# Kernel optimization log

Measured on AMD Instinct MI355X. Metric: run time of the kernel, lower is better.

Reference implementation:

```python
import jax, jax.numpy as jnp
import numpy as np

V, E, H, B, S = 50257, 1024, 1024, 32, 1024

def setup_inputs() -> dict:
    key = jax.random.key(0)
    ks = jax.random.split(key, 16)
    s = 0.02
    return {
        "word_inputs": jax.random.randint(ks[0], (B, 1), 0, V),
        "hidden": jax.random.normal(ks[1], (1, B, H), jnp.float32),
        "output_encoder": jax.random.normal(ks[2], (B, S, H), jnp.float32),
        "emb": jax.random.normal(ks[3], (V, E), jnp.float32) * 0.2,
        "W_a1": jax.random.normal(ks[4], (H, 2 * H), jnp.float32) * s,
        "b_a1": jnp.zeros((H,), jnp.float32),
        "W_a2": jax.random.normal(ks[5], (1, H), jnp.float32) * s,
        "b_a2": jnp.zeros((1,), jnp.float32),
        "W_c": jax.random.normal(ks[6], (H, 2 * H), jnp.float32) * s,
        "b_c": jnp.zeros((H,), jnp.float32),
        "W_ih": jax.random.normal(ks[7], (3 * H, E), jnp.float32) * s,
        "W_hh": jax.random.normal(ks[8], (3 * H, H), jnp.float32) * s,
        "b_ih": jnp.zeros((3 * H,), jnp.float32),
        "b_hh": jnp.zeros((3 * H,), jnp.float32),
        "W_fc": jax.random.normal(ks[9], (V, H), jnp.float32) * 0.2,
        "b_fc": jnp.zeros((V,), jnp.float32),
    }

def reference(word_inputs, hidden, output_encoder, emb, W_a1, b_a1, W_a2, b_a2,
              W_c, b_c, W_ih, W_hh, b_ih, b_hh, W_fc, b_fc):
    b, s, h = output_encoder.shape
    h_prev = hidden[0]                                      # [B,H]
    # Bahdanau additive attention, vectorized over all S timesteps
    eh = jnp.concatenate(
        [output_encoder, jnp.broadcast_to(h_prev[:, None, :], (b, s, h))],
        axis=-1)                                            # [B,S,2H]
    scores = jnp.tanh(jnp.einsum('bsk,hk->bsh', eh, W_a1) + b_a1)
    scores = (jnp.einsum('bsh,oh->bso', scores, W_a2) + b_a2)[..., 0]  # [B,S]
    attn = jax.nn.softmax(scores, axis=1)                   # [B,S]
    context = jnp.einsum('bs,bsh->bh', attn, output_encoder)  # [B,H]
    embedded = emb[word_inputs.reshape(-1)]                 # [B,E]
    ec = jnp.concatenate([embedded, context], axis=-1)      # [B,E+H]
    x = jax.nn.relu(ec @ W_c.T + b_c)                       # [B,H]
    # single-step GRU (PyTorch gate order: r, z, n)
    gi = x @ W_ih.T + b_ih                                  # [B,3H]
    gh = h_prev @ W_hh.T + b_hh                             # [B,3H]
    i_r, i_z, i_n = jnp.split(gi, 3, axis=-1)
    h_r, h_z, h_n = jnp.split(gh, 3, axis=-1)
    r = jax.nn.sigmoid(i_r + h_r)
    z = jax.nn.sigmoid(i_z + h_z)
    n = jnp.tanh(i_n + r * h_n)
    h_new = (1.0 - z) * n + z * h_prev                      # [B,H]
    out = jax.nn.relu(h_new) @ W_fc.T + b_fc                # [B,V]
    return out, h_new[None, :, :]
```

## Files before the change

### kernel.cpp

```cpp
#include <hip/hip_runtime.h>

#define B_  32
#define S_  1024
#define H_  1024
#define V_  50257

typedef __attribute__((ext_vector_type(8))) short bf16x8;
typedef __attribute__((ext_vector_type(4))) float f32x4;
typedef __attribute__((ext_vector_type(8))) unsigned short u16x8;

__device__ __forceinline__ unsigned short f2b(float f) {
  union { float f; unsigned u; } v; v.f = f;
  unsigned r = 0x7FFFu + ((v.u >> 16) & 1u);
  return (unsigned short)((v.u + r) >> 16);
}
__device__ __forceinline__ float b2f(unsigned short h) {
  union { unsigned u; float f; } v; v.u = ((unsigned)h) << 16;
  return v.f;
}

__device__ __forceinline__ void async16(void* lds, const void* g) {
  typedef __attribute__((address_space(3))) void as3_void;
  typedef __attribute__((address_space(1))) void as1_void;
  as3_void* l = (as3_void*)(unsigned)(unsigned long long)lds;
  const as1_void* s = (const as1_void*)(unsigned long long)g;
  __builtin_amdgcn_global_load_lds(s, l, 16, 0, 0);
}

__global__ void conv_f32_bf16(const float* __restrict__ src, unsigned short* __restrict__ dst) {
  size_t i = ((size_t)blockIdx.x * 256 + threadIdx.x) * 8;
  float4 v0 = *(const float4*)(src + i);
  float4 v1 = *(const float4*)(src + i + 4);
  u16x8 o;
  o[0]=f2b(v0.x); o[1]=f2b(v0.y); o[2]=f2b(v0.z); o[3]=f2b(v0.w);
  o[4]=f2b(v1.x); o[5]=f2b(v1.y); o[6]=f2b(v1.z); o[7]=f2b(v1.w);
  *(u16x8*)(dst + i) = o;
}

__global__ void wa1_prep_kernel(const float* __restrict__ wa1, const float* __restrict__ hidden,
                                const float* __restrict__ b_a1,
                                unsigned short* __restrict__ wa1_bf, float* __restrict__ part2) {
  int h = blockIdx.x;
  int tid = threadIdx.x;
  {
    int c = tid * 4;
    float4 v = *(const float4*)(wa1 + (size_t)h * 2048 + c);
    ushort4 o;
    o.x = f2b(v.x); o.y = f2b(v.y); o.z = f2b(v.z); o.w = f2b(v.w);
    *(ushort4*)(wa1_bf + (size_t)h * 1024 + c) = o;
  }
  __shared__ float wrow[H_];
  {
    int c = tid * 4;
    float4 v = *(const float4*)(wa1 + (size_t)h * 2048 + 1024 + c);
    wrow[c] = v.x; wrow[c+1] = v.y; wrow[c+2] = v.z; wrow[c+3] = v.w;
  }
  __syncthreads();
  int wave = tid >> 6, lane = tid & 63;
  float bias = b_a1[h];
  for (int bb = 0; bb < 8; ++bb) {
    int b = wave * 8 + bb;
    float acc = 0.f;
    for (int k = lane; k < H_; k += 64) acc += wrow[k] * hidden[b * H_ + k];
    #pragma unroll
    for (int off = 32; off; off >>= 1) acc += __shfl_xor(acc, off);
    if (lane == 0) part2[b * H_ + h] = acc + bias;
  }
}

#define NT_ 16
#define BAR()  __builtin_amdgcn_s_barrier()
#define SB0()  __builtin_amdgcn_sched_barrier(0)
#define VM6()  asm volatile("s_waitcnt vmcnt(6)" ::: "memory")
#define VM0()  asm volatile("s_waitcnt vmcnt(0)" ::: "memory")

#define LOADA(MH) { _Pragma("unroll") for (int m_ = 0; m_ < 4; ++m_) \
  { _Pragma("unroll") for (int ks_ = 0; ks_ < 2; ++ks_) { \
    int lr_ = (MH)*64 + m_*16 + l15; \
    int lin_ = lr_*128 + ks_*64 + l16*16; \
    int sw_ = lin_ ^ (((lin_>>9)&1)<<5); \
    af[m_][ks_] = *(const bf16x8*)(smem + buf*32768 + wr*16384 + sw_); } } }

#define LOADB() { _Pragma("unroll") for (int n_ = 0; n_ < 4; ++n_) \
  { _Pragma("unroll") for (int ks_ = 0; ks_ < 2; ++ks_) { \
    int lr_ = (wc&1)*64 + n_*16 + l15; \
    int lin_ = lr_*128 + ks_*64 + l16*16; \
    int sw_ = lin_ ^ (((lin_>>9)&1)<<5); \
    bfr[n_][ks_] = *(const bf16x8*)(smem + 65536 + buf*32768 + (wc>>1)*16384 + sw_); } } }

#define QUAD(MH, NH) { _Pragma("unroll") for (int m_ = 0; m_ < 4; ++m_) \
  { _Pragma("unroll") for (int n_ = 0; n_ < 2; ++n_) { \
    acc[(MH)*4+m_][(NH)*2+n_] = __builtin_amdgcn_mfma_f32_16x16x32_bf16(af[m_][0], bfr[(NH)*2+n_][0], acc[(MH)*4+m_][(NH)*2+n_], 0,0,0); \
    acc[(MH)*4+m_][(NH)*2+n_] = __builtin_amdgcn_mfma_f32_16x16x32_bf16(af[m_][1], bfr[(NH)*2+n_][1], acc[(MH)*4+m_][(NH)*2+n_], 0,0,0); } } }

#define PHASES(T, DO_B1, DO_T2, VMOP) { \
  const int buf = (T) & 1; \
  LOADA(0); LOADB(); \
  if (DO_B1) stB((T)+1, 1, buf^1); \
  BAR(); SB0(); \
  __builtin_amdgcn_s_setprio(1); QUAD(0,0); __builtin_amdgcn_s_setprio(0); \
  SB0(); BAR(); \
  if (DO_T2) stB((T)+2, 0, buf); \
  BAR(); SB0(); \
  __builtin_amdgcn_s_setprio(1); QUAD(0,1); __builtin_amdgcn_s_setprio(0); \
  SB0(); BAR(); \
  LOADA(1); \
  BAR(); SB0(); \
  __builtin_amdgcn_s_setprio(1); QUAD(1,1); __builtin_amdgcn_s_setprio(0); \
  SB0(); BAR(); \
  if (DO_T2) { stA((T)+2, 0, buf); stA((T)+2, 1, buf); } \
  VMOP; \
  BAR(); SB0(); \
  __builtin_amdgcn_s_setprio(1); QUAD(1,0); __builtin_amdgcn_s_setprio(0); \
  SB0(); BAR(); }

__global__ __launch_bounds__(512, 2) void scores_gemm8(
    const unsigned short* __restrict__ A,
    const unsigned short* __restrict__ Bm,
    const float* __restrict__ part2,
    const float* __restrict__ wa2,
    float* __restrict__ partials)
{
  extern __shared__ char smem[];
  const int tid = threadIdx.x;
  const int wave = tid >> 6, lane = tid & 63;
  const int wr = wave >> 2, wc = wave & 3;
  const int l15 = lane & 15, l16 = lane >> 4;
  const int bm = blockIdx.x, bn = blockIdx.y;

  const unsigned short* Abase = A  + (size_t)(bm * 256) * 1024;
  const unsigned short* Bbase = Bm + (size_t)(bn * 256) * 1024;

  const int Lc = tid * 16;
  const int Ls = Lc ^ (((Lc >> 9) & 1) << 5);
  const int sr = Ls >> 7;
  const int sk = (Ls & 127) >> 1;

  auto stA = [&](int t, int h, int db) {
    char* dst = smem + db * 32768 + h * 16384 + Lc;
    const unsigned short* src = Abase + (size_t)(h * 128 + sr) * 1024 + t * 64 + sk;
    async16(dst,        src);
    async16(dst + 8192, src + 64 * 1024);
  };
  auto stB = [&](int t, int h, int db) {
    char* dst = smem + 65536 + db * 32768 + h * 16384 + Lc;
    const unsigned short* src = Bbase + (size_t)(h * 128 + sr) * 1024 + t * 64 + sk;
    async16(dst,        src);
    async16(dst + 8192, src + 64 * 1024);
  };

  f32x4 acc[8][4];
  #pragma unroll
  for (int i = 0; i < 8; ++i)
    #pragma unroll
    for (int j = 0; j < 4; ++j) acc[i][j] = (f32x4){0.f, 0.f, 0.f, 0.f};
  bf16x8 af[4][2], bfr[4][2];

  stA(0, 0, 0); stA(0, 1, 0); stB(0, 0, 0); stB(0, 1, 0);
  stB(1, 0, 1); stA(1, 0, 1); stA(1, 1, 1);
  VM6();
  BAR();

  #pragma unroll 1
  for (int t = 0; t < NT_ - 2; ++t) PHASES(t, 1, 1, VM6());
  PHASES(NT_ - 2, 1, 0, VM0());
  PHASES(NT_ - 1, 0, 0, (void)0);

  const int b = bm >> 2;
  float w2[4], p2[4];
  #pragma unroll
  for (int ni = 0; ni < 4; ++ni) {
    int col = bn * 256 + wc * 64 + ni * 16 + l15;
    w2[ni] = wa2[col];
    p2[ni] = part2[b * H_ + col];
  }
  #pragma unroll
  for (int mi = 0; mi < 8; ++mi) {
    #pragma unroll
    for (int r = 0; r < 4; ++r) {
      float s = 0.f;
      #pragma unroll
      for (int ni = 0; ni < 4; ++ni)
        s += w2[ni] * tanhf(acc[mi][ni][r] + p2[ni]);
      s += __shfl_xor(s, 1); s += __shfl_xor(s, 2);
      s += __shfl_xor(s, 4); s += __shfl_xor(s, 8);
      if (l15 == 0) {
        int row = bm * 256 + wr * 128 + mi * 16 + l16 * 4 + r;
        partials[(size_t)row * 16 + bn * 4 + wc] = s;
      }
    }
  }
}

__global__ void softmax_kernel(const float* __restrict__ partials, const float* __restrict__ b_a2,
                               float* __restrict__ attn) {
  int b = blockIdx.x, s = threadIdx.x;
  int lane = s & 63, wid = s >> 6;
  const float4* p = (const float4*)(partials + (size_t)(b * S_ + s) * 16);
  float sc = b_a2[0];
  #pragma unroll
  for (int i = 0; i < 4; ++i) { float4 v = p[i]; sc += v.x + v.y + v.z + v.w; }
  __shared__ float rmax[16], rsum[16];
  float m = sc;
  #pragma unroll
  for (int off = 32; off; off >>= 1) m = fmaxf(m, __shfl_xor(m, off));
  if (lane == 0) rmax[wid] = m;
  __syncthreads();
  float M = rmax[0];
  #pragma unroll
  for (int i = 1; i < 16; ++i) M = fmaxf(M, rmax[i]);
  float e = expf(sc - M);
  float su = e;
  #pragma unroll
  for (int off = 32; off; off >>= 1) su += __shfl_xor(su, off);
  if (lane == 0) rsum[wid] = su;
  __syncthreads();
  float T = 0.f;
  #pragma unroll
  for (int i = 0; i < 16; ++i) T += rsum[i];
  attn[b * S_ + s] = e / T;
}

__global__ void ctx_partial_kernel(const unsigned short* __restrict__ encbf,
                                   const float* __restrict__ attn, float* __restrict__ ctxp) {
  int sc = blockIdx.x, b = blockIdx.y, t = threadIdx.x;
  int h4 = t * 4;
  float a0 = 0, a1 = 0, a2 = 0, a3 = 0;
  const unsigned short* base = encbf + (size_t)b * S_ * H_ + h4;
  const float* aw = attn + b * S_ + sc * 64;
  #pragma unroll 4
  for (int i = 0; i < 64; ++i) {
    float w = aw[i];
    ushort4 ev = *(const ushort4*)(base + (size_t)(sc * 64 + i) * H_);
    a0 += w * b2f(ev.x); a1 += w * b2f(ev.y); a2 += w * b2f(ev.z); a3 += w * b2f(ev.w);
  }
  float4 o = {a0, a1, a2, a3};
  *(float4*)(ctxp + (size_t)(sc * B_ + b) * H_ + h4) = o;
}

__global__ void prep_kernel(const float* __restrict__ ctxp, const float* __restrict__ emb,
                            const int* __restrict__ word, const float* __restrict__ hidden,
                            unsigned short* __restrict__ ec_bf, unsigned short* __restrict__ hprev_bf) {
  int b = blockIdx.x;
  int w = word[b];
  for (int h = threadIdx.x; h < H_; h += 256) {
    float c = 0.f;
    #pragma unroll
    for (int sc = 0; sc < 16; ++sc) c += ctxp[(size_t)(sc * B_ + b) * H_ + h];
    ec_bf[b * 2048 + 1024 + h] = f2b(c);
    ec_bf[b * 2048 + h] = f2b(emb[(size_t)w * H_ + h]);
    hprev_bf[b * H_ + h] = f2b(hidden[b * H_ + h]);
  }
}

__global__ __launch_bounds__(256) void skinny_gemm(
    const unsigned short* __restrict__ A, const float* __restrict__ Bw,
    float* __restrict__ C, const float* __restrict__ bias,
    int N, int K, int KC, int ldc, int mode)
{
  int n0 = blockIdx.x * 64;
  int kc = blockIdx.y;
  int wave = threadIdx.x >> 6, lane = threadIdx.x & 63;
  int l15 = lane & 15, l16 = lane >> 4;
  int col = n0 + wave * 16 + l15;
  int vclamp = col < N ? col : N - 1;
  const unsigned short* a0p = A + l15 * K + l16 * 8;
  const unsigned short* a1p = A + (16 + l15) * K + l16 * 8;
  const float* bp = Bw + (size_t)vclamp * K + l16 * 8;
  f32x4 acc0 = {0.f, 0.f, 0.f, 0.f}, acc1 = {0.f, 0.f, 0.f, 0.f};
  int k0 = kc * KC, k1 = (k0 + KC < K) ? (k0 + KC) : K;
  #pragma unroll 4
  for (int k = k0; k < k1; k += 32) {
    bf16x8 a0 = *(const bf16x8*)(a0p + k);
    bf16x8 a1 = *(const bf16x8*)(a1p + k);
    float4 bv0 = *(const float4*)(bp + k);
    float4 bv1 = *(const float4*)(bp + k + 4);
    bf16x8 bb;
    bb[0] = (short)f2b(bv0.x); bb[1] = (short)f2b(bv0.y);
    bb[2] = (short)f2b(bv0.z); bb[3] = (short)f2b(bv0.w);
    bb[4] = (short)f2b(bv1.x); bb[5] = (short)f2b(bv1.y);
    bb[6] = (short)f2b(bv1.z); bb[7] = (short)f2b(bv1.w);
    acc0 = __builtin_amdgcn_mfma_f32_16x16x32_bf16(a0, bb, acc0, 0, 0, 0);
    acc1 = __builtin_amdgcn_mfma_f32_16x16x32_bf16(a1, bb, acc1, 0, 0, 0);
  }
  if (col < N) {
    #pragma unroll
    for (int r = 0; r < 4; ++r) {
      int m = l16 * 4 + r;
      if (mode == 1) {
        float bv = bias[col];
        C[(size_t)m * ldc + col] = acc0[r] + bv;
        C[(size_t)(16 + m) * ldc + col] = acc1[r] + bv;
      } else {
        C[(size_t)(kc * 32 + m) * N + col] = acc0[r];
        C[(size_t)(kc * 32 + 16 + m) * N + col] = acc1[r];
      }
    }
  }
}

__global__ __launch_bounds__(256) void ihhh_gemm(
    const unsigned short* __restrict__ x_bf, const unsigned short* __restrict__ hprev_bf,
    const float* __restrict__ W_ih, const float* __restrict__ W_hh,
    float* __restrict__ gip, float* __restrict__ ghp)
{
  const unsigned short* A = blockIdx.z ? hprev_bf : x_bf;
  const float* Bw = blockIdx.z ? W_hh : W_ih;
  float* C = blockIdx.z ? ghp : gip;
  const int N = 3072, K = 1024, KC = 128;
  int n0 = blockIdx.x * 64;
  int kc = blockIdx.y;
  int wave = threadIdx.x >> 6, lane = threadIdx.x & 63;
  int l15 = lane & 15, l16 = lane >> 4;
  int col = n0 + wave * 16 + l15;
  const unsigned short* a0p = A + l15 * K + l16 * 8;
  const unsigned short* a1p = A + (16 + l15) * K + l16 * 8;
  const float* bp = Bw + (size_t)col * K + l16 * 8;
  f32x4 acc0 = {0.f, 0.f, 0.f, 0.f}, acc1 = {0.f, 0.f, 0.f, 0.f};
  int k0 = kc * KC;
  #pragma unroll 4
  for (int k = k0; k < k0 + KC; k += 32) {
    bf16x8 a0 = *(const bf16x8*)(a0p + k);
    bf16x8 a1 = *(const bf16x8*)(a1p + k);
    float4 bv0 = *(const float4*)(bp + k);
    float4 bv1 = *(const float4*)(bp + k + 4);
    bf16x8 bb;
    bb[0] = (short)f2b(bv0.x); bb[1] = (short)f2b(bv0.y);
    bb[2] = (short)f2b(bv0.z); bb[3] = (short)f2b(bv0.w);
    bb[4] = (short)f2b(bv1.x); bb[5] = (short)f2b(bv1.y);
    bb[6] = (short)f2b(bv1.z); bb[7] = (short)f2b(bv1.w);
    acc0 = __builtin_amdgcn_mfma_f32_16x16x32_bf16(a0, bb, acc0, 0, 0, 0);
    acc1 = __builtin_amdgcn_mfma_f32_16x16x32_bf16(a1, bb, acc1, 0, 0, 0);
  }
  #pragma unroll
  for (int r = 0; r < 4; ++r) {
    int m = l16 * 4 + r;
    C[(size_t)(kc * 32 + m) * N + col] = acc0[r];
    C[(size_t)(kc * 32 + 16 + m) * N + col] = acc1[r];
  }
}

__global__ void xfinish_kernel(const float* __restrict__ xp, const float* __restrict__ b_c,
                               unsigned short* __restrict__ x_bf) {
  int i = blockIdx.x * 256 + threadIdx.x;
  int b = i >> 10, h = i & 1023;
  float v = b_c[h];
  #pragma unroll
  for (int kc = 0; kc < 16; ++kc) v += xp[(size_t)(kc * B_ + b) * H_ + h];
  x_bf[i] = f2b(v > 0.f ? v : 0.f);
}

__global__ void gates_kernel(const float* __restrict__ gip, const float* __restrict__ ghp,
                             const float* __restrict__ b_ih, const float* __restrict__ b_hh,
                             const float* __restrict__ hidden, float* __restrict__ hnew_out,
                             unsigned short* __restrict__ hr_bf) {
  int i = blockIdx.x * 256 + threadIdx.x;
  int b = i >> 10, h = i & 1023;
  float g[6];
  #pragma unroll
  for (int t = 0; t < 3; ++t) {
    int j = h + t * H_;
    float vi = b_ih[j], vh = b_hh[j];
    #pragma unroll
    for (int kc = 0; kc < 8; ++kc) {
      vi += gip[(size_t)(kc * B_ + b) * 3072 + j];
      vh += ghp[(size_t)(kc * B_ + b) * 3072 + j];
    }
    g[t] = vi; g[3 + t] = vh;
  }
  float r = 1.f / (1.f + expf(-(g[0] + g[3])));
  float z = 1.f / (1.f + expf(-(g[1] + g[4])));
  float n = tanhf(g[2] + r * g[5]);
  float hv = (1.f - z) * n + z * hidden[i];
  hnew_out[i] = hv;
  hr_bf[i] = f2b(hv > 0.f ? hv : 0.f);
}

extern "C" void kernel_launch(void* const* d_in, const int* in_sizes, int n_in,
                              void* d_out, int out_size, void* d_ws, size_t ws_size,
                              hipStream_t stream) {
  const int*   word   = (const int*)  d_in[0];
  const float* hidden = (const float*)d_in[1];
  const float* enc    = (const float*)d_in[2];
  const float* emb    = (const float*)d_in[3];
  const float* W_a1   = (const float*)d_in[4];
  const float* b_a1   = (const float*)d_in[5];
  const float* W_a2   = (const float*)d_in[6];
  const float* b_a2   = (const float*)d_in[7];
  const float* W_c    = (const float*)d_in[8];
  const float* b_c    = (const float*)d_in[9];
  const float* W_ih   = (const float*)d_in[10];
  const float* W_hh   = (const float*)d_in[11];
  const float* b_ih   = (const float*)d_in[12];
  const float* b_hh   = (const float*)d_in[13];
  const float* W_fc   = (const float*)d_in[14];
  const float* b_fc   = (const float*)d_in[15];
  float* out = (float*)d_out;

  if (ws_size < 71892992ull) return;

  char* ws = (char*)d_ws;
  unsigned short* enc_bf   = (unsigned short*)(ws + 0);
  float*          gip      = (float*)         (ws + 0);
  float*          ghp      = (float*)         (ws + 3145728);
  unsigned short* wa1_bf   = (unsigned short*)(ws + 67108864);
  float*          xp       = (float*)         (ws + 67108864);
  float*          part2    = (float*)         (ws + 69206016);
  float*          partials = (float*)         (ws + 69337088);
  float*          ctxp     = (float*)         (ws + 69337088);
  float*          attn     = (float*)         (ws + 71434240);
  unsigned short* ec_bf    = (unsigned short*)(ws + 71565312);
  unsigned short* hprev_bf = (unsigned short*)(ws + 71696384);
  unsigned short* x_bf     = (unsigned short*)(ws + 71761920);
  unsigned short* hr_bf    = (unsigned short*)(ws + 71827456);

  hipFuncSetAttribute((const void*)scores_gemm8,
                      hipFuncAttributeMaxDynamicSharedMemorySize, 131072);

  conv_f32_bf16<<<dim3(16384), dim3(256), 0, stream>>>(enc, enc_bf);
  wa1_prep_kernel<<<dim3(1024), dim3(256), 0, stream>>>(W_a1, hidden, b_a1, wa1_bf, part2);
  scores_gemm8<<<dim3(128, 4), dim3(512), 131072, stream>>>(enc_bf, wa1_bf, part2, W_a2, partials);
  softmax_kernel<<<dim3(32), dim3(1024), 0, stream>>>(partials, b_a2, attn);
  ctx_partial_kernel<<<dim3(16, 32), dim3(256), 0, stream>>>(enc_bf, attn, ctxp);
  prep_kernel<<<dim3(32), dim3(256), 0, stream>>>(ctxp, emb, word, hidden, ec_bf, hprev_bf);
  skinny_gemm<<<dim3(16, 16), dim3(256), 0, stream>>>(ec_bf, W_c, xp, (const float*)nullptr,
                                                      1024, 2048, 128, 0, 0);
  xfinish_kernel<<<dim3(128), dim3(256), 0, stream>>>(xp, b_c, x_bf);
  ihhh_gemm<<<dim3(48, 8, 2), dim3(256), 0, stream>>>(x_bf, hprev_bf, W_ih, W_hh, gip, ghp);
  gates_kernel<<<dim3(128), dim3(256), 0, stream>>>(gip, ghp, b_ih, b_hh, hidden,
                                                    out + (size_t)B_ * V_, hr_bf);
  skinny_gemm<<<dim3(786, 1), dim3(256), 0, stream>>>(hr_bf, W_fc, out, b_fc,
                                                      V_, 1024, 1024, V_, 1);
}
```

Baseline: 288.2 us.

## Fuse prologue, softmax+context, operand prep and bias/relu into fewer GEMM kernels

Merges the encoder bf16 conversion and W_a1 prep into one launch. Softmax is recomputed inside each context block instead of running as a separate kernel. The context-partial reduction and embedding gather move into the W_c GEMM's LDS staging, and the W_c partial reduction with bias and relu moves into the ih/hh GEMM staging. This removes four kernel launches and their intermediate buffers, at the cost of repeating the softmax and partial-sum reductions in many blocks, which adds L2 read traffic.

```diff
diff --git a/kernel.cpp b/kernel.cpp
--- a/kernel.cpp
+++ b/kernel.cpp
@@ -27,21 +27,23 @@
   __builtin_amdgcn_global_load_lds(s, l, 16, 0, 0);
 }
 
-__global__ void conv_f32_bf16(const float* __restrict__ src, unsigned short* __restrict__ dst) {
-  size_t i = ((size_t)blockIdx.x * 256 + threadIdx.x) * 8;
-  float4 v0 = *(const float4*)(src + i);
-  float4 v1 = *(const float4*)(src + i + 4);
-  u16x8 o;
-  o[0]=f2b(v0.x); o[1]=f2b(v0.y); o[2]=f2b(v0.z); o[3]=f2b(v0.w);
-  o[4]=f2b(v1.x); o[5]=f2b(v1.y); o[6]=f2b(v1.z); o[7]=f2b(v1.w);
-  *(u16x8*)(dst + i) = o;
-}
-
-__global__ void wa1_prep_kernel(const float* __restrict__ wa1, const float* __restrict__ hidden,
+__global__ void prologue_kernel(const float* __restrict__ enc, unsigned short* __restrict__ enc_bf,
+                                const float* __restrict__ wa1, const float* __restrict__ hidden,
                                 const float* __restrict__ b_a1,
                                 unsigned short* __restrict__ wa1_bf, float* __restrict__ part2) {
-  int h = blockIdx.x;
+  __shared__ float wrow[H_];
   int tid = threadIdx.x;
+  if (blockIdx.x < 16384) {
+    size_t i = ((size_t)blockIdx.x * 256 + tid) * 8;
+    float4 v0 = *(const float4*)(enc + i);
+    float4 v1 = *(const float4*)(enc + i + 4);
+    u16x8 o;
+    o[0]=f2b(v0.x); o[1]=f2b(v0.y); o[2]=f2b(v0.z); o[3]=f2b(v0.w);
+    o[4]=f2b(v1.x); o[5]=f2b(v1.y); o[6]=f2b(v1.z); o[7]=f2b(v1.w);
+    *(u16x8*)(enc_bf + i) = o;
+    return;
+  }
+  int h = blockIdx.x - 16384;
   {
     int c = tid * 4;
     float4 v = *(const float4*)(wa1 + (size_t)h * 2048 + c);
@@ -49,7 +51,6 @@
     o.x = f2b(v.x); o.y = f2b(v.y); o.z = f2b(v.z); o.w = f2b(v.w);
     *(ushort4*)(wa1_bf + (size_t)h * 1024 + c) = o;
   }
-  __shared__ float wrow[H_];
   {
     int c = tid * 4;
     float4 v = *(const float4*)(wa1 + (size_t)h * 2048 + 1024 + c);
@@ -192,45 +193,44 @@
   }
 }
 
-__global__ void softmax_kernel(const float* __restrict__ partials, const float* __restrict__ b_a2,
-                               float* __restrict__ attn) {
-  int b = blockIdx.x, s = threadIdx.x;
-  int lane = s & 63, wid = s >> 6;
-  const float4* p = (const float4*)(partials + (size_t)(b * S_ + s) * 16);
-  float sc = b_a2[0];
-  #pragma unroll
-  for (int i = 0; i < 4; ++i) { float4 v = p[i]; sc += v.x + v.y + v.z + v.w; }
-  __shared__ float rmax[16], rsum[16];
-  float m = sc;
-  #pragma unroll
-  for (int off = 32; off; off >>= 1) m = fmaxf(m, __shfl_xor(m, off));
-  if (lane == 0) rmax[wid] = m;
-  __syncthreads();
-  float M = rmax[0];
-  #pragma unroll
-  for (int i = 1; i < 16; ++i) M = fmaxf(M, rmax[i]);
-  float e = expf(sc - M);
-  float su = e;
-  #pragma unroll
-  for (int off = 32; off; off >>= 1) su += __shfl_xor(su, off);
-  if (lane == 0) rsum[wid] = su;
-  __syncthreads();
-  float T = 0.f;
-  #pragma unroll
-  for (int i = 0; i < 16; ++i) T += rsum[i];
-  attn[b * S_ + s] = e / T;
-}
-
-__global__ void ctx_partial_kernel(const unsigned short* __restrict__ encbf,
-                                   const float* __restrict__ attn, float* __restrict__ ctxp) {
-  int sc = blockIdx.x, b = blockIdx.y, t = threadIdx.x;
-  int h4 = t * 4;
+__global__ __launch_bounds__(256) void smctx_kernel(
+    const float* __restrict__ partials, const unsigned short* __restrict__ encbf,
+    float* __restrict__ ctxp) {
+  int sc = blockIdx.x, b = blockIdx.y, tid = threadIdx.x;
+  int lane = tid & 63, wid = tid >> 6;
+  __shared__ float att[1024];
+  __shared__ float red[4];
+  float scv[4];
+  float mx = -1e30f;
+  #pragma unroll
+  for (int j = 0; j < 4; ++j) {
+    int r = tid * 4 + j;
+    const float4* p = (const float4*)(partials + ((size_t)b * 1024 + r) * 16);
+    float s = 0.f;
+    #pragma unroll
+    for (int i = 0; i < 4; ++i) { float4 v = p[i]; s += v.x + v.y + v.z + v.w; }
+    scv[j] = s; mx = fmaxf(mx, s);
+  }
+  #pragma unroll
+  for (int off = 32; off; off >>= 1) mx = fmaxf(mx, __shfl_xor(mx, off));
+  if (lane == 0) red[wid] = mx;
+  __syncthreads();
+  float M = fmaxf(fmaxf(red[0], red[1]), fmaxf(red[2], red[3]));
+  float ssum = 0.f;
+  #pragma unroll
+  for (int j = 0; j < 4; ++j) { float e = expf(scv[j] - M); att[tid*4+j] = e; ssum += e; }
+  #pragma unroll
+  for (int off = 32; off; off >>= 1) ssum += __shfl_xor(ssum, off);
+  __syncthreads();
+  if (lane == 0) red[wid] = ssum;
+  __syncthreads();
+  float inv = 1.f / (red[0] + red[1] + red[2] + red[3]);
+  int h4 = tid * 4;
   float a0 = 0, a1 = 0, a2 = 0, a3 = 0;
   const unsigned short* base = encbf + (size_t)b * S_ * H_ + h4;
-  const float* aw = attn + b * S_ + sc * 64;
   #pragma unroll 4
   for (int i = 0; i < 64; ++i) {
-    float w = aw[i];
+    float w = att[sc * 64 + i] * inv;
     ushort4 ev = *(const ushort4*)(base + (size_t)(sc * 64 + i) * H_);
     a0 += w * b2f(ev.x); a1 += w * b2f(ev.y); a2 += w * b2f(ev.z); a3 += w * b2f(ev.w);
   }
@@ -238,28 +238,161 @@
   *(float4*)(ctxp + (size_t)(sc * B_ + b) * H_ + h4) = o;
 }
 
-__global__ void prep_kernel(const float* __restrict__ ctxp, const float* __restrict__ emb,
-                            const int* __restrict__ word, const float* __restrict__ hidden,
-                            unsigned short* __restrict__ ec_bf, unsigned short* __restrict__ hprev_bf) {
-  int b = blockIdx.x;
-  int w = word[b];
-  for (int h = threadIdx.x; h < H_; h += 256) {
-    float c = 0.f;
-    #pragma unroll
-    for (int sc = 0; sc < 16; ++sc) c += ctxp[(size_t)(sc * B_ + b) * H_ + h];
-    ec_bf[b * 2048 + 1024 + h] = f2b(c);
-    ec_bf[b * 2048 + h] = f2b(emb[(size_t)w * H_ + h]);
-    hprev_bf[b * H_ + h] = f2b(hidden[b * H_ + h]);
-  }
-}
-
-__global__ __launch_bounds__(256) void skinny_gemm(
+__global__ __launch_bounds__(256) void wc_gemm(
+    const int* __restrict__ word, const float* __restrict__ emb,
+    const float* __restrict__ ctxp, const float* __restrict__ Wc,
+    float* __restrict__ xp) {
+  int nb = blockIdx.x, kc = blockIdx.y, tid = threadIdx.x;
+  __shared__ unsigned short A_lds[32][136];
+  {
+    int b = tid >> 3, cg = tid & 7;
+    int c0 = cg * 16;
+    if (kc < 8) {
+      int w = word[b];
+      const float* er = emb + (size_t)w * H_ + kc * 128 + c0;
+      #pragma unroll
+      for (int c = 0; c < 16; c += 4) {
+        float4 v = *(const float4*)(er + c);
+        ushort4 o; o.x = f2b(v.x); o.y = f2b(v.y); o.z = f2b(v.z); o.w = f2b(v.w);
+        *(ushort4*)&A_lds[b][c0 + c] = o;
+      }
+    } else {
+      int h0 = (kc - 8) * 128 + c0;
+      #pragma unroll
+      for (int c = 0; c < 16; c += 4) {
+        float s0 = 0, s1 = 0, s2 = 0, s3 = 0;
+        #pragma unroll
+        for (int sc = 0; sc < 16; ++sc) {
+          float4 v = *(const float4*)(ctxp + ((size_t)(sc * B_ + b)) * H_ + h0 + c);
+          s0 += v.x; s1 += v.y; s2 += v.z; s3 += v.w;
+        }
+        ushort4 o; o.x = f2b(s0); o.y = f2b(s1); o.z = f2b(s2); o.w = f2b(s3);
+        *(ushort4*)&A_lds[b][c0 + c] = o;
+      }
+    }
+  }
+  __syncthreads();
+  int wave = tid >> 6, lane = tid & 63, l15 = lane & 15, l16 = lane >> 4;
+  int col = nb * 64 + wave * 16 + l15;
+  const float* bp = Wc + (size_t)col * 2048 + kc * 128 + l16 * 8;
+  f32x4 acc0 = {0.f,0.f,0.f,0.f}, acc1 = {0.f,0.f,0.f,0.f};
+  #pragma unroll
+  for (int k = 0; k < 128; k += 32) {
+    bf16x8 a0 = *(const bf16x8*)&A_lds[l15][k + l16 * 8];
+    bf16x8 a1 = *(const bf16x8*)&A_lds[16 + l15][k + l16 * 8];
+    float4 bv0 = *(const float4*)(bp + k);
+    float4 bv1 = *(const float4*)(bp + k + 4);
+    bf16x8 bb;
+    bb[0] = (short)f2b(bv0.x); bb[1] = (short)f2b(bv0.y);
+    bb[2] = (short)f2b(bv0.z); bb[3] = (short)f2b(bv0.w);
+    bb[4] = (short)f2b(bv1.x); bb[5] = (short)f2b(bv1.y);
+    bb[6] = (short)f2b(bv1.z); bb[7] = (short)f2b(bv1.w);
+    acc0 = __builtin_amdgcn_mfma_f32_16x16x32_bf16(a0, bb, acc0, 0, 0, 0);
+    acc1 = __builtin_amdgcn_mfma_f32_16x16x32_bf16(a1, bb, acc1, 0, 0, 0);
+  }
+  #pragma unroll
+  for (int r = 0; r < 4; ++r) {
+    int m = l16 * 4 + r;
+    xp[(size_t)(kc * 32 + m) * H_ + col] = acc0[r];
+    xp[(size_t)(kc * 32 + 16 + m) * H_ + col] = acc1[r];
+  }
+}
+
+__global__ __launch_bounds__(256) void ihhh_gemm(
+    const float* __restrict__ xp, const float* __restrict__ b_c,
+    const float* __restrict__ hidden,
+    const float* __restrict__ W_ih, const float* __restrict__ W_hh,
+    float* __restrict__ gip, float* __restrict__ ghp) {
+  int nb = blockIdx.x, kc = blockIdx.y, z = blockIdx.z, tid = threadIdx.x;
+  __shared__ unsigned short A_lds[32][136];
+  {
+    int b = tid >> 3, cg = tid & 7;
+    int c0 = cg * 16;
+    int h0 = kc * 128 + c0;
+    if (z == 0) {
+      #pragma unroll
+      for (int c = 0; c < 16; c += 4) {
+        float4 bias = *(const float4*)(b_c + h0 + c);
+        float s0 = bias.x, s1 = bias.y, s2 = bias.z, s3 = bias.w;
+        #pragma unroll
+        for (int sc = 0; sc < 16; ++sc) {
+          float4 v = *(const float4*)(xp + ((size_t)(sc * B_ + b)) * H_ + h0 + c);
+          s0 += v.x; s1 += v.y; s2 += v.z; s3 += v.w;
+        }
+        ushort4 o;
+        o.x = f2b(fmaxf(s0, 0.f)); o.y = f2b(fmaxf(s1, 0.f));
+        o.z = f2b(fmaxf(s2, 0.f)); o.w = f2b(fmaxf(s3, 0.f));
+        *(ushort4*)&A_lds[b][c0 + c] = o;
+      }
+    } else {
+      #pragma unroll
+      for (int c = 0; c < 16; c += 4) {
+        float4 v = *(const float4*)(hidden + (size_t)b * H_ + h0 + c);
+        ushort4 o; o.x = f2b(v.x); o.y = f2b(v.y); o.z = f2b(v.z); o.w = f2b(v.w);
+        *(ushort4*)&A_lds[b][c0 + c] = o;
+      }
+    }
+  }
+  __syncthreads();
+  const float* Bw = z ? W_hh : W_ih;
+  float* C = z ? ghp : gip;
+  int wave = tid >> 6, lane = tid & 63, l15 = lane & 15, l16 = lane >> 4;
+  int col = nb * 64 + wave * 16 + l15;
+  const float* bp = Bw + (size_t)col * 1024 + kc * 128 + l16 * 8;
+  f32x4 acc0 = {0.f,0.f,0.f,0.f}, acc1 = {0.f,0.f,0.f,0.f};
+  #pragma unroll
+  for (int k = 0; k < 128; k += 32) {
+    bf16x8 a0 = *(const bf16x8*)&A_lds[l15][k + l16 * 8];
+    bf16x8 a1 = *(const bf16x8*)&A_lds[16 + l15][k + l16 * 8];
+    float4 bv0 = *(const float4*)(bp + k);
+    float4 bv1 = *(const float4*)(bp + k + 4);
+    bf16x8 bb;
+    bb[0] = (short)f2b(bv0.x); bb[1] = (short)f2b(bv0.y);
+    bb[2] = (short)f2b(bv0.z); bb[3] = (short)f2b(bv0.w);
+    bb[4] = (short)f2b(bv1.x); bb[5] = (short)f2b(bv1.y);
+    bb[6] = (short)f2b(bv1.z); bb[7] = (short)f2b(bv1.w);
+    acc0 = __builtin_amdgcn_mfma_f32_16x16x32_bf16(a0, bb, acc0, 0, 0, 0);
+    acc1 = __builtin_amdgcn_mfma_f32_16x16x32_bf16(a1, bb, acc1, 0, 0, 0);
+  }
+  #pragma unroll
+  for (int r = 0; r < 4; ++r) {
+    int m = l16 * 4 + r;
+    C[(size_t)(kc * 32 + m) * 3072 + col] = acc0[r];
+    C[(size_t)(kc * 32 + 16 + m) * 3072 + col] = acc1[r];
+  }
+}
+
+__global__ void gates_kernel(const float* __restrict__ gip, const float* __restrict__ ghp,
+                             const float* __restrict__ b_ih, const float* __restrict__ b_hh,
+                             const float* __restrict__ hidden, float* __restrict__ hnew_out,
+                             unsigned short* __restrict__ hr_bf) {
+  int i = blockIdx.x * 256 + threadIdx.x;
+  int b = i >> 10, h = i & 1023;
+  float g[6];
+  #pragma unroll
+  for (int t = 0; t < 3; ++t) {
+    int j = h + t * H_;
+    float vi = b_ih[j], vh = b_hh[j];
+    #pragma unroll
+    for (int kc = 0; kc < 8; ++kc) {
+      vi += gip[(size_t)(kc * B_ + b) * 3072 + j];
+      vh += ghp[(size_t)(kc * B_ + b) * 3072 + j];
+    }
+    g[t] = vi; g[3 + t] = vh;
+  }
+  float r = 1.f / (1.f + expf(-(g[0] + g[3])));
+  float z = 1.f / (1.f + expf(-(g[1] + g[4])));
+  float n = tanhf(g[2] + r * g[5]);
+  float hv = (1.f - z) * n + z * hidden[i];
+  hnew_out[i] = hv;
+  hr_bf[i] = f2b(hv > 0.f ? hv : 0.f);
+}
+
+__global__ __launch_bounds__(256) void fc_gemm(
     const unsigned short* __restrict__ A, const float* __restrict__ Bw,
-    float* __restrict__ C, const float* __restrict__ bias,
-    int N, int K, int KC, int ldc, int mode)
-{
+    float* __restrict__ C, const float* __restrict__ bias) {
+  const int N = V_, K = 1024;
   int n0 = blockIdx.x * 64;
-  int kc = blockIdx.y;
   int wave = threadIdx.x >> 6, lane = threadIdx.x & 63;
   int l15 = lane & 15, l16 = lane >> 4;
   int col = n0 + wave * 16 + l15;
@@ -267,10 +400,9 @@
   const unsigned short* a0p = A + l15 * K + l16 * 8;
   const unsigned short* a1p = A + (16 + l15) * K + l16 * 8;
   const float* bp = Bw + (size_t)vclamp * K + l16 * 8;
-  f32x4 acc0 = {0.f, 0.f, 0.f, 0.f}, acc1 = {0.f, 0.f, 0.f, 0.f};
-  int k0 = kc * KC, k1 = (k0 + KC < K) ? (k0 + KC) : K;
+  f32x4 acc0 = {0.f,0.f,0.f,0.f}, acc1 = {0.f,0.f,0.f,0.f};
   #pragma unroll 4
-  for (int k = k0; k < k1; k += 32) {
+  for (int k = 0; k < K; k += 32) {
     bf16x8 a0 = *(const bf16x8*)(a0p + k);
     bf16x8 a1 = *(const bf16x8*)(a1p + k);
     float4 bv0 = *(const float4*)(bp + k);
@@ -284,96 +416,14 @@
     acc1 = __builtin_amdgcn_mfma_f32_16x16x32_bf16(a1, bb, acc1, 0, 0, 0);
   }
   if (col < N) {
+    float bv = bias[col];
     #pragma unroll
     for (int r = 0; r < 4; ++r) {
       int m = l16 * 4 + r;
-      if (mode == 1) {
-        float bv = bias[col];
-        C[(size_t)m * ldc + col] = acc0[r] + bv;
-        C[(size_t)(16 + m) * ldc + col] = acc1[r] + bv;
-      } else {
-        C[(size_t)(kc * 32 + m) * N + col] = acc0[r];
-        C[(size_t)(kc * 32 + 16 + m) * N + col] = acc1[r];
-      }
+      C[(size_t)m * N + col] = acc0[r] + bv;
+      C[(size_t)(16 + m) * N + col] = acc1[r] + bv;
     }
   }
-}
-
-__global__ __launch_bounds__(256) void ihhh_gemm(
-    const unsigned short* __restrict__ x_bf, const unsigned short* __restrict__ hprev_bf,
-    const float* __restrict__ W_ih, const float* __restrict__ W_hh,
-    float* __restrict__ gip, float* __restrict__ ghp)
-{
-  const unsigned short* A = blockIdx.z ? hprev_bf : x_bf;
-  const float* Bw = blockIdx.z ? W_hh : W_ih;
-  float* C = blockIdx.z ? ghp : gip;
-  const int N = 3072, K = 1024, KC = 128;
-  int n0 = blockIdx.x * 64;
-  int kc = blockIdx.y;
-  int wave = threadIdx.x >> 6, lane = threadIdx.x & 63;
-  int l15 = lane & 15, l16 = lane >> 4;
-  int col = n0 + wave * 16 + l15;
-  const unsigned short* a0p = A + l15 * K + l16 * 8;
-  const unsigned short* a1p = A + (16 + l15) * K + l16 * 8;
-  const float* bp = Bw + (size_t)col * K + l16 * 8;
-  f32x4 acc0 = {0.f, 0.f, 0.f, 0.f}, acc1 = {0.f, 0.f, 0.f, 0.f};
-  int k0 = kc * KC;
-  #pragma unroll 4
-  for (int k = k0; k < k0 + KC; k += 32) {
-    bf16x8 a0 = *(const bf16x8*)(a0p + k);
-    bf16x8 a1 = *(const bf16x8*)(a1p + k);
-    float4 bv0 = *(const float4*)(bp + k);
-    float4 bv1 = *(const float4*)(bp + k + 4);
-    bf16x8 bb;
-    bb[0] = (short)f2b(bv0.x); bb[1] = (short)f2b(bv0.y);
-    bb[2] = (short)f2b(bv0.z); bb[3] = (short)f2b(bv0.w);
-    bb[4] = (short)f2b(bv1.x); bb[5] = (short)f2b(bv1.y);
-    bb[6] = (short)f2b(bv1.z); bb[7] = (short)f2b(bv1.w);
-    acc0 = __builtin_amdgcn_mfma_f32_16x16x32_bf16(a0, bb, acc0, 0, 0, 0);
-    acc1 = __builtin_amdgcn_mfma_f32_16x16x32_bf16(a1, bb, acc1, 0, 0, 0);
-  }
-  #pragma unroll
-  for (int r = 0; r < 4; ++r) {
-    int m = l16 * 4 + r;
-    C[(size_t)(kc * 32 + m) * N + col] = acc0[r];
-    C[(size_t)(kc * 32 + 16 + m) * N + col] = acc1[r];
-  }
-}
-
-__global__ void xfinish_kernel(const float* __restrict__ xp, const float* __restrict__ b_c,
-                               unsigned short* __restrict__ x_bf) {
-  int i = blockIdx.x * 256 + threadIdx.x;
-  int b = i >> 10, h = i & 1023;
-  float v = b_c[h];
-  #pragma unroll
-  for (int kc = 0; kc < 16; ++kc) v += xp[(size_t)(kc * B_ + b) * H_ + h];
-  x_bf[i] = f2b(v > 0.f ? v : 0.f);
-}
-
-__global__ void gates_kernel(const float* __restrict__ gip, const float* __restrict__ ghp,
-                             const float* __restrict__ b_ih, const float* __restrict__ b_hh,
-                             const float* __restrict__ hidden, float* __restrict__ hnew_out,
-                             unsigned short* __restrict__ hr_bf) {
-  int i = blockIdx.x * 256 + threadIdx.x;
-  int b = i >> 10, h = i & 1023;
-  float g[6];
-  #pragma unroll
-  for (int t = 0; t < 3; ++t) {
-    int j = h + t * H_;
-    float vi = b_ih[j], vh = b_hh[j];
-    #pragma unroll
-    for (int kc = 0; kc < 8; ++kc) {
-      vi += gip[(size_t)(kc * B_ + b) * 3072 + j];
-      vh += ghp[(size_t)(kc * B_ + b) * 3072 + j];
-    }
-    g[t] = vi; g[3 + t] = vh;
-  }
-  float r = 1.f / (1.f + expf(-(g[0] + g[3])));
-  float z = 1.f / (1.f + expf(-(g[1] + g[4])));
-  float n = tanhf(g[2] + r * g[5]);
-  float hv = (1.f - z) * n + z * hidden[i];
-  hnew_out[i] = hv;
-  hr_bf[i] = f2b(hv > 0.f ? hv : 0.f);
 }
 
 extern "C" void kernel_launch(void* const* d_in, const int* in_sizes, int n_in,
@@ -386,9 +436,8 @@
   const float* W_a1   = (const float*)d_in[4];
   const float* b_a1   = (const float*)d_in[5];
   const float* W_a2   = (const float*)d_in[6];
-  const float* b_a2   = (const float*)d_in[7];
+  const float* b_c    = (const float*)d_in[9];
   const float* W_c    = (const float*)d_in[8];
-  const float* b_c    = (const float*)d_in[9];
   const float* W_ih   = (const float*)d_in[10];
   const float* W_hh   = (const float*)d_in[11];
   const float* b_ih   = (const float*)d_in[12];
@@ -397,7 +446,7 @@
   const float* b_fc   = (const float*)d_in[15];
   float* out = (float*)d_out;
 
-  if (ws_size < 71892992ull) return;
+  if (ws_size < 73596928ull) return;
 
   char* ws = (char*)d_ws;
   unsigned short* enc_bf   = (unsigned short*)(ws + 0);
@@ -407,28 +456,19 @@
   float*          xp       = (float*)         (ws + 67108864);
   float*          part2    = (float*)         (ws + 69206016);
   float*          partials = (float*)         (ws + 69337088);
-  float*          ctxp     = (float*)         (ws + 69337088);
-  float*          attn     = (float*)         (ws + 71434240);
-  unsigned short* ec_bf    = (unsigned short*)(ws + 71565312);
-  unsigned short* hprev_bf = (unsigned short*)(ws + 71696384);
-  unsigned short* x_bf     = (unsigned short*)(ws + 71761920);
-  unsigned short* hr_bf    = (unsigned short*)(ws + 71827456);
+  float*          ctxp     = (float*)         (ws + 71434240);
+  unsigned short* hr_bf    = (unsigned short*)(ws + 73531392);
 
   hipFuncSetAttribute((const void*)scores_gemm8,
                       hipFuncAttributeMaxDynamicSharedMemorySize, 131072);
 
-  conv_f32_bf16<<<dim3(16384), dim3(256), 0, stream>>>(enc, enc_bf);
-  wa1_prep_kernel<<<dim3(1024), dim3(256), 0, stream>>>(W_a1, hidden, b_a1, wa1_bf, part2);
+  prologue_kernel<<<dim3(17408), dim3(256), 0, stream>>>(enc, enc_bf, W_a1, hidden, b_a1,
+                                                         wa1_bf, part2);
   scores_gemm8<<<dim3(128, 4), dim3(512), 131072, stream>>>(enc_bf, wa1_bf, part2, W_a2, partials);
-  softmax_kernel<<<dim3(32), dim3(1024), 0, stream>>>(partials, b_a2, attn);
-  ctx_partial_kernel<<<dim3(16, 32), dim3(256), 0, stream>>>(enc_bf, attn, ctxp);
-  prep_kernel<<<dim3(32), dim3(256), 0, stream>>>(ctxp, emb, word, hidden, ec_bf, hprev_bf);
-  skinny_gemm<<<dim3(16, 16), dim3(256), 0, stream>>>(ec_bf, W_c, xp, (const float*)nullptr,
-                                                      1024, 2048, 128, 0, 0);
-  xfinish_kernel<<<dim3(128), dim3(256), 0, stream>>>(xp, b_c, x_bf);
-  ihhh_gemm<<<dim3(48, 8, 2), dim3(256), 0, stream>>>(x_bf, hprev_bf, W_ih, W_hh, gip, ghp);
+  smctx_kernel<<<dim3(16, 32), dim3(256), 0, stream>>>(partials, enc_bf, ctxp);
+  wc_gemm<<<dim3(16, 16), dim3(256), 0, stream>>>(word, emb, ctxp, W_c, xp);
+  ihhh_gemm<<<dim3(48, 8, 2), dim3(256), 0, stream>>>(xp, b_c, hidden, W_ih, W_hh, gip, ghp);
   gates_kernel<<<dim3(128), dim3(256), 0, stream>>>(gip, ghp, b_ih, b_hh, hidden,
                                                     out + (size_t)B_ * V_, hr_bf);
-  skinny_gemm<<<dim3(786, 1), dim3(256), 0, stream>>>(hr_bf, W_fc, out, b_fc,
-                                                      V_, 1024, 1024, V_, 1);
-}
+  fc_gemm<<<dim3(786), dim3(256), 0, stream>>>(hr_bf, W_fc, out, b_fc);
+}
```

New measurement: 293.8 us. Within noise of the previous version (+2.0%).
